# Performance work log

Measured on AMD Instinct MI355X. Metric: run time of the kernel, lower is better.

Reference implementation:

```python
import jax, jax.numpy as jnp
import numpy as np


def _rgcn_layer(x, rel, adj, W, b):
    # x: [B, N, De], rel: [B, R, Dr], adj: [B, R, N, N]
    # Torch loop: for each r, bmm(adj[:, r], cat([x, rel[:, r] broadcast], -1)), then cat over r.
    B, N, De = x.shape
    R, Dr = rel.shape[1], rel.shape[2]
    h = jnp.concatenate(
        [jnp.broadcast_to(x[:, None], (B, R, N, De)),
         jnp.broadcast_to(rel[:, :, None], (B, R, N, Dr))],
        axis=-1)                                   # [B, R, N, De+Dr]
    # supports, with relation axis placed before features to match torch cat order
    s = jnp.einsum('brmn,brnd->bmrd', adj, h)      # [B, N, R, De+Dr]
    s = s.reshape(B, N, R * (De + Dr))             # [B, N, R*(De+Dr)]
    return s @ W.T + b                             # [B, N, out_dim]


def setup_inputs() -> dict:
    key = jax.random.key(0)
    ks = jax.random.split(key, 6)
    B, N, R = 16, 1024, 10
    De, Dr, H = 64, 32, 64
    cat_in = (De + Dr) * R  # 960
    node_features = jax.random.normal(ks[0], (B, N, De), dtype=jnp.float32)
    relation_features = jax.random.normal(ks[1], (B, R, Dr), dtype=jnp.float32)
    adj = jax.random.uniform(ks[2], (B, R, N, N), dtype=jnp.float32)
    scale0 = np.sqrt(6.0 / (cat_in + H)).astype(np.float32)  # xavier_uniform
    W0 = jax.random.uniform(ks[3], (H, cat_in), minval=-scale0, maxval=scale0, dtype=jnp.float32)
    b0 = jnp.zeros((H,), dtype=jnp.float32)
    W1 = jax.random.uniform(ks[4], (H, cat_in), minval=-scale0, maxval=scale0, dtype=jnp.float32)
    b1 = jnp.zeros((H,), dtype=jnp.float32)
    return {"node_features": node_features, "relation_features": relation_features,
            "adj": adj, "W0": W0, "b0": b0, "W1": W1, "b1": b1}


def reference(node_features, relation_features, adj, W0, b0, W1, b1):
    # StackedRelationalGraphConvolution.forward, 2 layers, no highway,
    # real_valued_graph=False (ReLU), dropout_rate=0 (inference no-op).
    x = jax.nn.relu(_rgcn_layer(node_features, relation_features, adj, W0, b0))
    x = jax.nn.relu(_rgcn_layer(x, relation_features, adj, W1, b1))
    return x
```

## Files before the change

### kernel.cpp

```cpp
#include <hip/hip_runtime.h>
#include <hip/hip_bf16.h>


typedef __bf16 bf16x8 __attribute__((ext_vector_type(8)));
typedef float  f32x4  __attribute__((ext_vector_type(4)));
typedef float  f32x8  __attribute__((ext_vector_type(8)));

__global__ void rgcn_c(const float* __restrict__ rel, const float* __restrict__ W,
                       float* __restrict__ cbuf) {
    const int h = threadIdx.x;
    const int b = blockIdx.x / 10;
    const int r = blockIdx.x % 10;
    const float* rp = rel + (size_t)(b * 10 + r) * 32;
    const float* wp = W + (size_t)h * 960 + r * 96 + 64;
    float acc = 0.f;
#pragma unroll
    for (int d = 0; d < 32; ++d) acc += rp[d] * wp[d];
    cbuf[(size_t)(b * 10 + r) * 64 + h] = acc;
}

__global__ __launch_bounds__(256)
void rgcn_prep(const float* __restrict__ x, const float* __restrict__ W,
               const float* __restrict__ cbuf, __bf16* __restrict__ yt) {
    const int n = blockIdx.x * 256 + threadIdx.x;
    const int r = blockIdx.y;
    const int b = blockIdx.z;

    float xr[64];
    const float* xp = x + ((size_t)b * 1024 + n) * 64;
#pragma unroll
    for (int j = 0; j < 16; ++j) {
        const float4 v = *(const float4*)(xp + j * 4);
        xr[j * 4 + 0] = v.x; xr[j * 4 + 1] = v.y;
        xr[j * 4 + 2] = v.z; xr[j * 4 + 3] = v.w;
    }

    const int br = b * 10 + r;
    const float* wbase = W + r * 96;
    const float* cb = cbuf + (size_t)br * 64;
    __bf16* yb = yt + (size_t)br * 64 * 1024 + n;

    for (int h = 0; h < 64; ++h) {
        float acc = cb[h];
        const float* wr = wbase + (size_t)h * 960;
#pragma unroll
        for (int d = 0; d < 64; ++d) acc += xr[d] * wr[d];
        yb[(size_t)h * 1024] = (__bf16)acc;
    }
}

template<int NR, bool FUSE>
__global__ __launch_bounds__(256, 2)
void rgcn_main(const float* __restrict__ adj, const __bf16* __restrict__ yt,
               float* __restrict__ partial, const float* __restrict__ bias,
               float* __restrict__ dst) {
    const int mtile = blockIdx.x, rg = blockIdx.y, b = blockIdx.z;
    const int w = threadIdx.x >> 6, lane = threadIdx.x & 63;
    const int g = lane >> 4, lm = lane & 15;
    const int mbase = mtile * 128 + w * 32;

    f32x4 acc[2][4] = {};

    for (int rr = 0; rr < NR; ++rr) {
        const int br = b * 10 + rg * NR + rr;
        const float*  a0 = adj + (((size_t)br * 1024 + mbase + lm) << 10) + g * 8;
        const __bf16* y0 = yt  + (((size_t)br * 64 + lm) << 10) + g * 8;
        for (int n0 = 0; n0 < 1024; n0 += 32) {
            const f32x8 v0 = *(const f32x8*)(a0 + n0);
            const f32x8 v1 = *(const f32x8*)(a0 + (16 << 10) + n0);
            bf16x8 av0, av1;
#pragma unroll
            for (int j = 0; j < 8; ++j) {
                av0[j] = (__bf16)v0[j];
                av1[j] = (__bf16)v1[j];
            }
#pragma unroll
            for (int hf = 0; hf < 4; ++hf) {
                const bf16x8 bv = *(const bf16x8*)(y0 + (size_t)hf * 16 * 1024 + n0);
                acc[0][hf] = __builtin_amdgcn_mfma_f32_16x16x32_bf16(av0, bv, acc[0][hf], 0, 0, 0);
                acc[1][hf] = __builtin_amdgcn_mfma_f32_16x16x32_bf16(av1, bv, acc[1][hf], 0, 0, 0);
            }
        }
    }

    if (FUSE) {
        float bvals[4];
#pragma unroll
        for (int hf = 0; hf < 4; ++hf) bvals[hf] = bias[hf * 16 + lm];
        float* db = dst + ((size_t)b * 1024 + mbase) * 64;
#pragma unroll
        for (int mf = 0; mf < 2; ++mf)
#pragma unroll
            for (int hf = 0; hf < 4; ++hf)
#pragma unroll
                for (int reg = 0; reg < 4; ++reg) {
                    const int m = mf * 16 + g * 4 + reg;
                    const int h = hf * 16 + lm;
                    db[(size_t)m * 64 + h] = fmaxf(acc[mf][hf][reg] + bvals[hf], 0.f);
                }
    } else {
        float* pb = partial + (((size_t)rg * 16 + b) * 1024 + mbase) * 64;
#pragma unroll
        for (int mf = 0; mf < 2; ++mf)
#pragma unroll
            for (int hf = 0; hf < 4; ++hf)
#pragma unroll
                for (int reg = 0; reg < 4; ++reg) {
                    const int m = mf * 16 + g * 4 + reg;
                    const int h = hf * 16 + lm;
                    pb[(size_t)m * 64 + h] = acc[mf][hf][reg];
                }
    }
}

__global__ __launch_bounds__(256)
void rgcn_epi(const float* __restrict__ partial, const float* __restrict__ bias,
              float* __restrict__ dst) {
    const size_t i = (size_t)blockIdx.x * 256 + threadIdx.x;
    const size_t off = i * 4;
    f32x4 s = {};
#pragma unroll
    for (int p = 0; p < 5; ++p)
        s += *(const f32x4*)(partial + (size_t)p * 1048576 + off);
    const f32x4 bv = *(const f32x4*)(bias + (int)(off & 63));
#pragma unroll
    for (int j = 0; j < 4; ++j) s[j] = fmaxf(s[j] + bv[j], 0.f);
    *(f32x4*)(dst + off) = s;
}

extern "C" void kernel_launch(void* const* d_in, const int* in_sizes, int n_in,
                              void* d_out, int out_size, void* d_ws, size_t ws_size,
                              hipStream_t stream) {
    const float* x   = (const float*)d_in[0];
    const float* rel = (const float*)d_in[1];
    const float* adj = (const float*)d_in[2];
    const float* W0  = (const float*)d_in[3];
    const float* b0  = (const float*)d_in[4];
    const float* W1  = (const float*)d_in[5];
    const float* b1  = (const float*)d_in[6];
    float* out = (float*)d_out;

    char* ws = (char*)d_ws;
    __bf16* Yt   = (__bf16*)ws;
    float* cbuf  = (float*)(ws + 20971520);
    float* x2    = (float*)(ws + 21012480);
    float* part  = (float*)(ws + 25206784);
    const bool big = ws_size >= 46178304;

    for (int layer = 0; layer < 2; ++layer) {
        const float* xin  = layer ? x2 : x;
        const float* W    = layer ? W1 : W0;
        const float* bias = layer ? b1 : b0;
        float* dst        = layer ? out : x2;

        rgcn_c<<<160, 64, 0, stream>>>(rel, W, cbuf);
        rgcn_prep<<<dim3(4, 10, 16), 256, 0, stream>>>(xin, W, cbuf, Yt);
        if (big) {
            rgcn_main<2, false><<<dim3(8, 5, 16), 256, 0, stream>>>(adj, Yt, part, nullptr, nullptr);
            rgcn_epi<<<1024, 256, 0, stream>>>(part, bias, dst);
        } else {
            rgcn_main<10, true><<<dim3(8, 1, 16), 256, 0, stream>>>(adj, Yt, nullptr, bias, dst);
        }
    }
}
```

Before: 569.7 us.

## Split main GEMM per relation, prefetch adj with nontemporal loads, fuse bias kernel

Folds the relation-bias kernel into the prep kernel through shared memory, which removes one launch per layer. The main kernel now assigns one relation per block, giving a 160x8 grid instead of 8x5x16. Each block writes its own partial, and the epilogue sums 10 partials instead of 5. The adj stream is software-prefetched one step ahead with nontemporal loads, and the occupancy hint rises to 4 blocks per CU. The cost is a larger partial buffer that needs more workspace, plus extra epilogue traffic.

```diff
diff --git a/kernel.cpp b/kernel.cpp
--- a/kernel.cpp
+++ b/kernel.cpp
@@ -4,28 +4,26 @@
 
 typedef __bf16 bf16x8 __attribute__((ext_vector_type(8)));
 typedef float  f32x4  __attribute__((ext_vector_type(4)));
-typedef float  f32x8  __attribute__((ext_vector_type(8)));
-
-__global__ void rgcn_c(const float* __restrict__ rel, const float* __restrict__ W,
-                       float* __restrict__ cbuf) {
-    const int h = threadIdx.x;
-    const int b = blockIdx.x / 10;
-    const int r = blockIdx.x % 10;
-    const float* rp = rel + (size_t)(b * 10 + r) * 32;
-    const float* wp = W + (size_t)h * 960 + r * 96 + 64;
-    float acc = 0.f;
-#pragma unroll
-    for (int d = 0; d < 32; ++d) acc += rp[d] * wp[d];
-    cbuf[(size_t)(b * 10 + r) * 64 + h] = acc;
-}
 
 __global__ __launch_bounds__(256)
-void rgcn_prep(const float* __restrict__ x, const float* __restrict__ W,
-               const float* __restrict__ cbuf, __bf16* __restrict__ yt) {
+void rgcn_prep(const float* __restrict__ x, const float* __restrict__ rel,
+               const float* __restrict__ W, __bf16* __restrict__ yt) {
+    const int r = blockIdx.y, b = blockIdx.z;
+    const int br = b * 10 + r;
+
+    __shared__ float csh[64];
+    if (threadIdx.x < 64) {
+        const int h = threadIdx.x;
+        const float* rp = rel + (size_t)br * 32;
+        const float* wp = W + (size_t)h * 960 + r * 96 + 64;
+        float a = 0.f;
+#pragma unroll
+        for (int d = 0; d < 32; ++d) a += rp[d] * wp[d];
+        csh[h] = a;
+    }
+    __syncthreads();
+
     const int n = blockIdx.x * 256 + threadIdx.x;
-    const int r = blockIdx.y;
-    const int b = blockIdx.z;
-
     float xr[64];
     const float* xp = x + ((size_t)b * 1024 + n) * 64;
 #pragma unroll
@@ -35,59 +33,100 @@
         xr[j * 4 + 2] = v.z; xr[j * 4 + 3] = v.w;
     }
 
-    const int br = b * 10 + r;
     const float* wbase = W + r * 96;
-    const float* cb = cbuf + (size_t)br * 64;
-    __bf16* yb = yt + (size_t)br * 64 * 1024 + n;
-
+    __bf16* yb = yt + ((size_t)br << 16) + n;
     for (int h = 0; h < 64; ++h) {
-        float acc = cb[h];
+        float acc = csh[h];
         const float* wr = wbase + (size_t)h * 960;
 #pragma unroll
         for (int d = 0; d < 64; ++d) acc += xr[d] * wr[d];
-        yb[(size_t)h * 1024] = (__bf16)acc;
+        yb[(size_t)h << 10] = (__bf16)acc;
     }
 }
 
-template<int NR, bool FUSE>
-__global__ __launch_bounds__(256, 2)
+template<bool FUSE>
+__global__ __launch_bounds__(256, 4)
 void rgcn_main(const float* __restrict__ adj, const __bf16* __restrict__ yt,
                float* __restrict__ partial, const float* __restrict__ bias,
                float* __restrict__ dst) {
-    const int mtile = blockIdx.x, rg = blockIdx.y, b = blockIdx.z;
     const int w = threadIdx.x >> 6, lane = threadIdx.x & 63;
     const int g = lane >> 4, lm = lane & 15;
-    const int mbase = mtile * 128 + w * 32;
 
-    f32x4 acc[2][4] = {};
+#define LDNT(p, o) __builtin_nontemporal_load((const f32x4*)((p) + (o)))
 
-    for (int rr = 0; rr < NR; ++rr) {
-        const int br = b * 10 + rg * NR + rr;
+    if constexpr (!FUSE) {
+        const int br = blockIdx.x;
+        const int mtile = blockIdx.y;
+        const int mbase = mtile * 128 + w * 32;
+
         const float*  a0 = adj + (((size_t)br * 1024 + mbase + lm) << 10) + g * 8;
-        const __bf16* y0 = yt  + (((size_t)br * 64 + lm) << 10) + g * 8;
-        for (int n0 = 0; n0 < 1024; n0 += 32) {
-            const f32x8 v0 = *(const f32x8*)(a0 + n0);
-            const f32x8 v1 = *(const f32x8*)(a0 + (16 << 10) + n0);
-            bf16x8 av0, av1;
+        const float*  a1 = a0 + (16 << 10);
+        const __bf16* y0 = yt + ((size_t)br << 16) + (lm << 10) + g * 8;
+
+        f32x4 acc[2][4] = {};
+        f32x4 c00 = LDNT(a0, 0), c01 = LDNT(a0, 4);
+        f32x4 c10 = LDNT(a1, 0), c11 = LDNT(a1, 4);
+
+#define STEP(N0)                                                               \
+        {                                                                      \
+            bf16x8 av0, av1;                                                   \
+            _Pragma("unroll")                                                  \
+            for (int j = 0; j < 4; ++j) {                                      \
+                av0[j] = (__bf16)c00[j]; av0[4 + j] = (__bf16)c01[j];          \
+                av1[j] = (__bf16)c10[j]; av1[4 + j] = (__bf16)c11[j];          \
+            }                                                                  \
+            _Pragma("unroll")                                                  \
+            for (int hf = 0; hf < 4; ++hf) {                                   \
+                const bf16x8 bv = *(const bf16x8*)(y0 + hf * 16384 + (N0));    \
+                acc[0][hf] = __builtin_amdgcn_mfma_f32_16x16x32_bf16(av0, bv, acc[0][hf], 0, 0, 0); \
+                acc[1][hf] = __builtin_amdgcn_mfma_f32_16x16x32_bf16(av1, bv, acc[1][hf], 0, 0, 0); \
+            }                                                                  \
+        }
+
+        for (int n0 = 0; n0 < 992; n0 += 32) {
+            const f32x4 p00 = LDNT(a0, n0 + 32), p01 = LDNT(a0, n0 + 36);
+            const f32x4 p10 = LDNT(a1, n0 + 32), p11 = LDNT(a1, n0 + 36);
+            STEP(n0)
+            c00 = p00; c01 = p01; c10 = p10; c11 = p11;
+        }
+        STEP(992)
+
+        float* pb = partial + ((size_t)br << 16);
 #pragma unroll
-            for (int j = 0; j < 8; ++j) {
-                av0[j] = (__bf16)v0[j];
-                av1[j] = (__bf16)v1[j];
+        for (int mf = 0; mf < 2; ++mf)
+#pragma unroll
+            for (int hf = 0; hf < 4; ++hf)
+#pragma unroll
+                for (int reg = 0; reg < 4; ++reg) {
+                    const int m = mbase + mf * 16 + g * 4 + reg;
+                    const int h = hf * 16 + lm;
+                    pb[((size_t)m << 6) + h] = acc[mf][hf][reg];
+                }
+    } else {
+        const int b = blockIdx.x;
+        const int mtile = blockIdx.y;
+        const int mbase = mtile * 128 + w * 32;
+
+        f32x4 acc[2][4] = {};
+        for (int r = 0; r < 10; ++r) {
+            const int br = b * 10 + r;
+            const float*  a0 = adj + (((size_t)br * 1024 + mbase + lm) << 10) + g * 8;
+            const float*  a1 = a0 + (16 << 10);
+            const __bf16* y0 = yt + ((size_t)br << 16) + (lm << 10) + g * 8;
+            f32x4 c00 = LDNT(a0, 0), c01 = LDNT(a0, 4);
+            f32x4 c10 = LDNT(a1, 0), c11 = LDNT(a1, 4);
+            for (int n0 = 0; n0 < 992; n0 += 32) {
+                const f32x4 p00 = LDNT(a0, n0 + 32), p01 = LDNT(a0, n0 + 36);
+                const f32x4 p10 = LDNT(a1, n0 + 32), p11 = LDNT(a1, n0 + 36);
+                STEP(n0)
+                c00 = p00; c01 = p01; c10 = p10; c11 = p11;
             }
-#pragma unroll
-            for (int hf = 0; hf < 4; ++hf) {
-                const bf16x8 bv = *(const bf16x8*)(y0 + (size_t)hf * 16 * 1024 + n0);
-                acc[0][hf] = __builtin_amdgcn_mfma_f32_16x16x32_bf16(av0, bv, acc[0][hf], 0, 0, 0);
-                acc[1][hf] = __builtin_amdgcn_mfma_f32_16x16x32_bf16(av1, bv, acc[1][hf], 0, 0, 0);
-            }
+            STEP(992)
         }
-    }
-
-    if (FUSE) {
         float bvals[4];
 #pragma unroll
         for (int hf = 0; hf < 4; ++hf) bvals[hf] = bias[hf * 16 + lm];
-        float* db = dst + ((size_t)b * 1024 + mbase) * 64;
+        float* db = dst + (((size_t)b * 1024 + mbase) << 6);
 #pragma unroll
         for (int mf = 0; mf < 2; ++mf)
 #pragma unroll
@@ -96,21 +135,11 @@
                 for (int reg = 0; reg < 4; ++reg) {
                     const int m = mf * 16 + g * 4 + reg;
                     const int h = hf * 16 + lm;
-                    db[(size_t)m * 64 + h] = fmaxf(acc[mf][hf][reg] + bvals[hf], 0.f);
-                }
-    } else {
-        float* pb = partial + (((size_t)rg * 16 + b) * 1024 + mbase) * 64;
-#pragma unroll
-        for (int mf = 0; mf < 2; ++mf)
-#pragma unroll
-            for (int hf = 0; hf < 4; ++hf)
-#pragma unroll
-                for (int reg = 0; reg < 4; ++reg) {
-                    const int m = mf * 16 + g * 4 + reg;
-                    const int h = hf * 16 + lm;
-                    pb[(size_t)m * 64 + h] = acc[mf][hf][reg];
+                    db[((size_t)m << 6) + h] = fmaxf(acc[mf][hf][reg] + bvals[hf], 0.f);
                 }
     }
+#undef STEP
+#undef LDNT
 }
 
 __global__ __launch_bounds__(256)
@@ -118,10 +147,12 @@
               float* __restrict__ dst) {
     const size_t i = (size_t)blockIdx.x * 256 + threadIdx.x;
     const size_t off = i * 4;
+    const size_t b = off >> 16;
+    const size_t inner = off & 65535;
     f32x4 s = {};
 #pragma unroll
-    for (int p = 0; p < 5; ++p)
-        s += *(const f32x4*)(partial + (size_t)p * 1048576 + off);
+    for (int p = 0; p < 10; ++p)
+        s += *(const f32x4*)(partial + (((b * 10 + p) << 16) | inner));
     const f32x4 bv = *(const f32x4*)(bias + (int)(off & 63));
 #pragma unroll
     for (int j = 0; j < 4; ++j) s[j] = fmaxf(s[j] + bv[j], 0.f);
@@ -141,11 +172,10 @@
     float* out = (float*)d_out;
 
     char* ws = (char*)d_ws;
-    __bf16* Yt   = (__bf16*)ws;
-    float* cbuf  = (float*)(ws + 20971520);
-    float* x2    = (float*)(ws + 21012480);
-    float* part  = (float*)(ws + 25206784);
-    const bool big = ws_size >= 46178304;
+    __bf16* Yt  = (__bf16*)ws;
+    float* x2   = (float*)(ws + 20971520);
+    float* part = (float*)(ws + 25165824);
+    const bool big = ws_size >= 67108864;
 
     for (int layer = 0; layer < 2; ++layer) {
         const float* xin  = layer ? x2 : x;
@@ -153,13 +183,12 @@
         const float* bias = layer ? b1 : b0;
         float* dst        = layer ? out : x2;
 
-        rgcn_c<<<160, 64, 0, stream>>>(rel, W, cbuf);
-        rgcn_prep<<<dim3(4, 10, 16), 256, 0, stream>>>(xin, W, cbuf, Yt);
+        rgcn_prep<<<dim3(4, 10, 16), 256, 0, stream>>>(xin, rel, W, Yt);
         if (big) {
-            rgcn_main<2, false><<<dim3(8, 5, 16), 256, 0, stream>>>(adj, Yt, part, nullptr, nullptr);
+            rgcn_main<false><<<dim3(160, 8), 256, 0, stream>>>(adj, Yt, part, nullptr, nullptr);
             rgcn_epi<<<1024, 256, 0, stream>>>(part, bias, dst);
         } else {
-            rgcn_main<10, true><<<dim3(8, 1, 16), 256, 0, stream>>>(adj, Yt, nullptr, bias, dst);
+            rgcn_main<true><<<dim3(16, 8), 256, 0, stream>>>(adj, Yt, nullptr, bias, dst);
         }
     }
 }
```

Result: slower. 631.3 us (+10.8%).

## Cache bf16 fragment-layout copy of adjacency in layer one for reuse in layer two

Applied to the files above, without the earlier changes.

During the first layer, the main kernel writes the bf16-converted adjacency tiles to workspace in the exact per-lane MFMA fragment order. The second layer's main kernel then reads these half-size, contiguous fragments instead of re-reading and re-converting the fp32 adjacency. The separate relation-bias kernel is also folded into the prep kernel through shared memory, which removes one launch per layer. The trade-off is roughly 335 MB of extra writes in layer one and a much larger workspace requirement; if the workspace is too small, execution falls back to the fused per-layer path.

```diff
diff --git a/kernel.cpp b/kernel.cpp
--- a/kernel.cpp
+++ b/kernel.cpp
@@ -6,26 +6,25 @@
 typedef float  f32x4  __attribute__((ext_vector_type(4)));
 typedef float  f32x8  __attribute__((ext_vector_type(8)));
 
-__global__ void rgcn_c(const float* __restrict__ rel, const float* __restrict__ W,
-                       float* __restrict__ cbuf) {
-    const int h = threadIdx.x;
-    const int b = blockIdx.x / 10;
-    const int r = blockIdx.x % 10;
-    const float* rp = rel + (size_t)(b * 10 + r) * 32;
-    const float* wp = W + (size_t)h * 960 + r * 96 + 64;
-    float acc = 0.f;
-#pragma unroll
-    for (int d = 0; d < 32; ++d) acc += rp[d] * wp[d];
-    cbuf[(size_t)(b * 10 + r) * 64 + h] = acc;
-}
-
 __global__ __launch_bounds__(256)
-void rgcn_prep(const float* __restrict__ x, const float* __restrict__ W,
-               const float* __restrict__ cbuf, __bf16* __restrict__ yt) {
+void rgcn_prep(const float* __restrict__ x, const float* __restrict__ rel,
+               const float* __restrict__ W, __bf16* __restrict__ yt) {
+    const int r = blockIdx.y, b = blockIdx.z;
+    const int br = b * 10 + r;
+
+    __shared__ float csh[64];
+    if (threadIdx.x < 64) {
+        const int h = threadIdx.x;
+        const float* rp = rel + (size_t)br * 32;
+        const float* wp = W + (size_t)h * 960 + r * 96 + 64;
+        float a = 0.f;
+#pragma unroll
+        for (int d = 0; d < 32; ++d) a += rp[d] * wp[d];
+        csh[h] = a;
+    }
+    __syncthreads();
+
     const int n = blockIdx.x * 256 + threadIdx.x;
-    const int r = blockIdx.y;
-    const int b = blockIdx.z;
-
     float xr[64];
     const float* xp = x + ((size_t)b * 1024 + n) * 64;
 #pragma unroll
@@ -35,25 +34,20 @@
         xr[j * 4 + 2] = v.z; xr[j * 4 + 3] = v.w;
     }
 
-    const int br = b * 10 + r;
     const float* wbase = W + r * 96;
-    const float* cb = cbuf + (size_t)br * 64;
-    __bf16* yb = yt + (size_t)br * 64 * 1024 + n;
-
+    __bf16* yb = yt + ((size_t)br << 16) + n;
     for (int h = 0; h < 64; ++h) {
-        float acc = cb[h];
+        float acc = csh[h];
         const float* wr = wbase + (size_t)h * 960;
 #pragma unroll
         for (int d = 0; d < 64; ++d) acc += xr[d] * wr[d];
-        yb[(size_t)h * 1024] = (__bf16)acc;
-    }
-}
-
-template<int NR, bool FUSE>
+        yb[(size_t)h << 10] = (__bf16)acc;
+    }
+}
+
 __global__ __launch_bounds__(256, 2)
-void rgcn_main(const float* __restrict__ adj, const __bf16* __restrict__ yt,
-               float* __restrict__ partial, const float* __restrict__ bias,
-               float* __restrict__ dst) {
+void rgcn_main1(const float* __restrict__ adj, const __bf16* __restrict__ yt,
+                float* __restrict__ partial, __bf16* __restrict__ abf) {
     const int mtile = blockIdx.x, rg = blockIdx.y, b = blockIdx.z;
     const int w = threadIdx.x >> 6, lane = threadIdx.x & 63;
     const int g = lane >> 4, lm = lane & 15;
@@ -61,8 +55,98 @@
 
     f32x4 acc[2][4] = {};
 
-    for (int rr = 0; rr < NR; ++rr) {
-        const int br = b * 10 + rg * NR + rr;
+    for (int rr = 0; rr < 2; ++rr) {
+        const int br = b * 10 + rg * 2 + rr;
+        const float*  a0 = adj + (((size_t)br * 1024 + mbase + lm) << 10) + g * 8;
+        const __bf16* y0 = yt  + (((size_t)br * 64 + lm) << 10) + g * 8;
+        __bf16* ab = abf + ((size_t)(br * 8 + mtile) << 17);
+
+        for (int n0 = 0; n0 < 1024; n0 += 32) {
+            const f32x8 v0 = *(const f32x8*)(a0 + n0);
+            const f32x8 v1 = *(const f32x8*)(a0 + (16 << 10) + n0);
+            bf16x8 av0, av1;
+#pragma unroll
+            for (int j = 0; j < 8; ++j) {
+                av0[j] = (__bf16)v0[j];
+                av1[j] = (__bf16)v1[j];
+            }
+            const int c = n0 >> 5;
+            *(bf16x8*)(ab + ((c * 8 + w * 2 + 0) << 9) + lane * 8) = av0;
+            *(bf16x8*)(ab + ((c * 8 + w * 2 + 1) << 9) + lane * 8) = av1;
+#pragma unroll
+            for (int hf = 0; hf < 4; ++hf) {
+                const bf16x8 bv = *(const bf16x8*)(y0 + hf * 16384 + n0);
+                acc[0][hf] = __builtin_amdgcn_mfma_f32_16x16x32_bf16(av0, bv, acc[0][hf], 0, 0, 0);
+                acc[1][hf] = __builtin_amdgcn_mfma_f32_16x16x32_bf16(av1, bv, acc[1][hf], 0, 0, 0);
+            }
+        }
+    }
+
+    float* pb = partial + (((size_t)rg * 16 + b) << 16) + (size_t)mbase * 64;
+#pragma unroll
+    for (int mf = 0; mf < 2; ++mf)
+#pragma unroll
+        for (int hf = 0; hf < 4; ++hf)
+#pragma unroll
+            for (int reg = 0; reg < 4; ++reg) {
+                const int m = mf * 16 + g * 4 + reg;
+                const int h = hf * 16 + lm;
+                pb[((size_t)m << 6) + h] = acc[mf][hf][reg];
+            }
+}
+
+__global__ __launch_bounds__(256, 2)
+void rgcn_main2(const __bf16* __restrict__ abf, const __bf16* __restrict__ yt,
+                float* __restrict__ partial) {
+    const int mtile = blockIdx.x, rg = blockIdx.y, b = blockIdx.z;
+    const int w = threadIdx.x >> 6, lane = threadIdx.x & 63;
+    const int g = lane >> 4, lm = lane & 15;
+    const int mbase = mtile * 128 + w * 32;
+
+    f32x4 acc[2][4] = {};
+
+    for (int rr = 0; rr < 2; ++rr) {
+        const int br = b * 10 + rg * 2 + rr;
+        const __bf16* y0 = yt + (((size_t)br * 64 + lm) << 10) + g * 8;
+        const __bf16* ab = abf + ((size_t)(br * 8 + mtile) << 17);
+
+        for (int n0 = 0; n0 < 1024; n0 += 32) {
+            const int c = n0 >> 5;
+            const bf16x8 av0 = *(const bf16x8*)(ab + ((c * 8 + w * 2 + 0) << 9) + lane * 8);
+            const bf16x8 av1 = *(const bf16x8*)(ab + ((c * 8 + w * 2 + 1) << 9) + lane * 8);
+#pragma unroll
+            for (int hf = 0; hf < 4; ++hf) {
+                const bf16x8 bv = *(const bf16x8*)(y0 + hf * 16384 + n0);
+                acc[0][hf] = __builtin_amdgcn_mfma_f32_16x16x32_bf16(av0, bv, acc[0][hf], 0, 0, 0);
+                acc[1][hf] = __builtin_amdgcn_mfma_f32_16x16x32_bf16(av1, bv, acc[1][hf], 0, 0, 0);
+            }
+        }
+    }
+
+    float* pb = partial + (((size_t)rg * 16 + b) << 16) + (size_t)mbase * 64;
+#pragma unroll
+    for (int mf = 0; mf < 2; ++mf)
+#pragma unroll
+        for (int hf = 0; hf < 4; ++hf)
+#pragma unroll
+            for (int reg = 0; reg < 4; ++reg) {
+                const int m = mf * 16 + g * 4 + reg;
+                const int h = hf * 16 + lm;
+                pb[((size_t)m << 6) + h] = acc[mf][hf][reg];
+            }
+}
+
+__global__ __launch_bounds__(256, 2)
+void rgcn_mainF(const float* __restrict__ adj, const __bf16* __restrict__ yt,
+                const float* __restrict__ bias, float* __restrict__ dst) {
+    const int mtile = blockIdx.x, b = blockIdx.z;
+    const int w = threadIdx.x >> 6, lane = threadIdx.x & 63;
+    const int g = lane >> 4, lm = lane & 15;
+    const int mbase = mtile * 128 + w * 32;
+
+    f32x4 acc[2][4] = {};
+    for (int r = 0; r < 10; ++r) {
+        const int br = b * 10 + r;
         const float*  a0 = adj + (((size_t)br * 1024 + mbase + lm) << 10) + g * 8;
         const __bf16* y0 = yt  + (((size_t)br * 64 + lm) << 10) + g * 8;
         for (int n0 = 0; n0 < 1024; n0 += 32) {
@@ -70,47 +154,29 @@
             const f32x8 v1 = *(const f32x8*)(a0 + (16 << 10) + n0);
             bf16x8 av0, av1;
 #pragma unroll
-            for (int j = 0; j < 8; ++j) {
-                av0[j] = (__bf16)v0[j];
-                av1[j] = (__bf16)v1[j];
-            }
+            for (int j = 0; j < 8; ++j) { av0[j] = (__bf16)v0[j]; av1[j] = (__bf16)v1[j]; }
 #pragma unroll
             for (int hf = 0; hf < 4; ++hf) {
-                const bf16x8 bv = *(const bf16x8*)(y0 + (size_t)hf * 16 * 1024 + n0);
+                const bf16x8 bv = *(const bf16x8*)(y0 + hf * 16384 + n0);
                 acc[0][hf] = __builtin_amdgcn_mfma_f32_16x16x32_bf16(av0, bv, acc[0][hf], 0, 0, 0);
                 acc[1][hf] = __builtin_amdgcn_mfma_f32_16x16x32_bf16(av1, bv, acc[1][hf], 0, 0, 0);
             }
         }
     }
-
-    if (FUSE) {
-        float bvals[4];
-#pragma unroll
-        for (int hf = 0; hf < 4; ++hf) bvals[hf] = bias[hf * 16 + lm];
-        float* db = dst + ((size_t)b * 1024 + mbase) * 64;
-#pragma unroll
-        for (int mf = 0; mf < 2; ++mf)
-#pragma unroll
-            for (int hf = 0; hf < 4; ++hf)
-#pragma unroll
-                for (int reg = 0; reg < 4; ++reg) {
-                    const int m = mf * 16 + g * 4 + reg;
-                    const int h = hf * 16 + lm;
-                    db[(size_t)m * 64 + h] = fmaxf(acc[mf][hf][reg] + bvals[hf], 0.f);
-                }
-    } else {
-        float* pb = partial + (((size_t)rg * 16 + b) * 1024 + mbase) * 64;
-#pragma unroll
-        for (int mf = 0; mf < 2; ++mf)
-#pragma unroll
-            for (int hf = 0; hf < 4; ++hf)
-#pragma unroll
-                for (int reg = 0; reg < 4; ++reg) {
-                    const int m = mf * 16 + g * 4 + reg;
-                    const int h = hf * 16 + lm;
-                    pb[(size_t)m * 64 + h] = acc[mf][hf][reg];
-                }
-    }
+    float bvals[4];
+#pragma unroll
+    for (int hf = 0; hf < 4; ++hf) bvals[hf] = bias[hf * 16 + lm];
+    float* db = dst + (((size_t)b * 1024 + mbase)) * 64;
+#pragma unroll
+    for (int mf = 0; mf < 2; ++mf)
+#pragma unroll
+        for (int hf = 0; hf < 4; ++hf)
+#pragma unroll
+            for (int reg = 0; reg < 4; ++reg) {
+                const int m = mf * 16 + g * 4 + reg;
+                const int h = hf * 16 + lm;
+                db[((size_t)m << 6) + h] = fmaxf(acc[mf][hf][reg] + bvals[hf], 0.f);
+            }
 }
 
 __global__ __launch_bounds__(256)
@@ -142,24 +208,26 @@
 
     char* ws = (char*)d_ws;
     __bf16* Yt   = (__bf16*)ws;
-    float* cbuf  = (float*)(ws + 20971520);
-    float* x2    = (float*)(ws + 21012480);
-    float* part  = (float*)(ws + 25206784);
-    const bool big = ws_size >= 46178304;
-
-    for (int layer = 0; layer < 2; ++layer) {
-        const float* xin  = layer ? x2 : x;
-        const float* W    = layer ? W1 : W0;
-        const float* bias = layer ? b1 : b0;
-        float* dst        = layer ? out : x2;
-
-        rgcn_c<<<160, 64, 0, stream>>>(rel, W, cbuf);
-        rgcn_prep<<<dim3(4, 10, 16), 256, 0, stream>>>(xin, W, cbuf, Yt);
-        if (big) {
-            rgcn_main<2, false><<<dim3(8, 5, 16), 256, 0, stream>>>(adj, Yt, part, nullptr, nullptr);
-            rgcn_epi<<<1024, 256, 0, stream>>>(part, bias, dst);
-        } else {
-            rgcn_main<10, true><<<dim3(8, 1, 16), 256, 0, stream>>>(adj, Yt, nullptr, bias, dst);
-        }
-    }
-}
+    float*  x2   = (float*)(ws + 20971520);
+    float*  part = (float*)(ws + 25165824);
+    __bf16* abf  = (__bf16*)(ws + 46137344);
+    const bool big = ws_size >= 381681664u;
+
+    if (big) {
+        rgcn_prep<<<dim3(4, 10, 16), 256, 0, stream>>>(x, rel, W0, Yt);
+        rgcn_main1<<<dim3(8, 5, 16), 256, 0, stream>>>(adj, Yt, part, abf);
+        rgcn_epi<<<1024, 256, 0, stream>>>(part, b0, x2);
+        rgcn_prep<<<dim3(4, 10, 16), 256, 0, stream>>>(x2, rel, W1, Yt);
+        rgcn_main2<<<dim3(8, 5, 16), 256, 0, stream>>>(abf, Yt, part);
+        rgcn_epi<<<1024, 256, 0, stream>>>(part, b1, out);
+    } else {
+        for (int layer = 0; layer < 2; ++layer) {
+            const float* xin  = layer ? x2 : x;
+            const float* W    = layer ? W1 : W0;
+            const float* bias = layer ? b1 : b0;
+            float* dst        = layer ? out : x2;
+            rgcn_prep<<<dim3(4, 10, 16), 256, 0, stream>>>(xin, rel, W, Yt);
+            rgcn_mainF<<<dim3(8, 1, 16), 256, 0, stream>>>(adj, Yt, bias, dst);
+        }
+    }
+}
```

After: 629.7 us. 1.11x slower.
